# Kernel tuning notes

Measured on AMD Instinct MI355X. Metric: run time of the kernel, lower is better.

## Reference

```python
import jax, jax.numpy as jnp
import numpy as np

B, D_IN, T = 16, 1024, 4096
CB_SIZE, CB_DIM = 1024, 8
EPS = 1e-12  # F.normalize eps


def _wn_weight(v, g):
    # weight_norm over dim=0: per-output-row normalization. v: [out, in], g: [out]
    return g[:, None] * v / jnp.linalg.norm(v, axis=1, keepdims=True)


def setup_inputs() -> dict:
    key = jax.random.key(0)
    ks = jax.random.split(key, 8)
    z = jax.random.normal(ks[0], (B, D_IN, T), dtype=jnp.float32)
    in_v = jax.random.normal(ks[1], (CB_DIM, D_IN), dtype=jnp.float32) * 0.02
    in_g = jnp.linalg.norm(in_v, axis=1)  # weight_norm init: g = ||v||
    in_b = jnp.zeros((CB_DIM,), dtype=jnp.float32)
    out_v = jax.random.normal(ks[2], (D_IN, CB_DIM), dtype=jnp.float32) * 0.02
    out_g = jnp.linalg.norm(out_v, axis=1)
    out_b = jnp.zeros((D_IN,), dtype=jnp.float32)
    codebook = jax.random.normal(ks[3], (CB_SIZE, CB_DIM), dtype=jnp.float32)
    return {"z": z, "in_v": in_v, "in_g": in_g, "in_b": in_b,
            "out_v": out_v, "out_g": out_g, "out_b": out_b, "codebook": codebook}


def reference(z, in_v, in_g, in_b, out_v, out_g, out_b, codebook):
    # in_proj: 1x1 weight-normed conv, z: [B, D_IN, T] -> z_e: [B, CB_DIM, T]
    w_in = _wn_weight(in_v, in_g)
    z_e = jnp.einsum('od,bdt->bot', w_in, z) + in_b[None, :, None]

    # decode_latents: (b t) d tokens, L2-normalize, cosine distance, argmin
    enc = z_e.transpose(0, 2, 1).reshape(-1, CB_DIM)              # [(B*T), CB_DIM]
    enc_n = enc / jnp.maximum(jnp.linalg.norm(enc, axis=1, keepdims=True), EPS)
    cb_n = codebook / jnp.maximum(jnp.linalg.norm(codebook, axis=1, keepdims=True), EPS)
    dist = (jnp.sum(enc_n ** 2, axis=1, keepdims=True)
            - 2.0 * enc_n @ cb_n.T
            + jnp.sum(cb_n ** 2, axis=1)[None, :])                # [(B*T), CB_SIZE]
    indices = jnp.argmax(-dist, axis=1).reshape(B, T)             # argmin of dist
    z_q = codebook[indices].transpose(0, 2, 1)                    # [B, CB_DIM, T]

    commitment_loss = jnp.mean((z_e - jax.lax.stop_gradient(z_q)) ** 2, axis=(1, 2))
    codebook_loss = jnp.mean((z_q - jax.lax.stop_gradient(z_e)) ** 2, axis=(1, 2))

    # straight-through estimator
    z_q_st = z_e + jax.lax.stop_gradient(z_q - z_e)

    # out_proj: 1x1 weight-normed conv back to input_dim
    w_out = _wn_weight(out_v, out_g)
    z_out = jnp.einsum('od,bdt->bot', w_out, z_q_st) + out_b[None, :, None]
    return (z_out, commitment_loss, codebook_loss, indices, z_e)
```

## Files before the change

### kernel.cpp

```cpp
#include <hip/hip_runtime.h>
#include <math.h>


namespace {
constexpr int kB  = 16;
constexpr int kD  = 1024;
constexpr int kT  = 4096;
constexpr int kCB = 1024;
constexpr int kC  = 8;
constexpr float kEps = 1e-12f;

constexpr size_t N_ZOUT    = (size_t)kB * kD * kT;
constexpr size_t OFF_COMMIT = N_ZOUT;
constexpr size_t OFF_CBL    = OFF_COMMIT + kB;
constexpr size_t OFF_IDX    = OFF_CBL + kB;
constexpr size_t OFF_ZE     = OFF_IDX + (size_t)kB * kT;
}

__global__ void vq_prep(const float* __restrict__ in_v, const float* __restrict__ in_g,
                        const float* __restrict__ out_v, const float* __restrict__ out_g,
                        const float* __restrict__ cb,
                        float* __restrict__ w_in_t, float* __restrict__ w_out_t,
                        float* __restrict__ cb_n_t)
{
    __shared__ float red[4];
    const int blk = blockIdx.x;
    const int tid = threadIdx.x;
    if (blk < 8) {
        const int o = blk;
        float ss = 0.f;
        for (int d = tid; d < kD; d += 256) {
            float v = in_v[o * kD + d];
            ss = fmaf(v, v, ss);
        }
        #pragma unroll
        for (int off = 32; off; off >>= 1) ss += __shfl_xor(ss, off);
        if ((tid & 63) == 0) red[tid >> 6] = ss;
        __syncthreads();
        const float scale = in_g[o] / sqrtf(red[0] + red[1] + red[2] + red[3]);
        for (int d = tid; d < kD; d += 256)
            w_in_t[d * kC + o] = scale * in_v[o * kD + d];
    } else if (blk < 12) {
        const int r = (blk - 8) * 256 + tid;
        float4 a = reinterpret_cast<const float4*>(cb)[2 * r];
        float4 b = reinterpret_cast<const float4*>(cb)[2 * r + 1];
        float n = sqrtf(a.x*a.x + a.y*a.y + a.z*a.z + a.w*a.w +
                        b.x*b.x + b.y*b.y + b.z*b.z + b.w*b.w);
        float s = 1.f / fmaxf(n, kEps);
        a.x *= s; a.y *= s; a.z *= s; a.w *= s;
        b.x *= s; b.y *= s; b.z *= s; b.w *= s;
        reinterpret_cast<float4*>(cb_n_t)[2 * r]     = a;
        reinterpret_cast<float4*>(cb_n_t)[2 * r + 1] = b;
    } else {
        const int r = (blk - 12) * 256 + tid;
        float4 a = reinterpret_cast<const float4*>(out_v)[2 * r];
        float4 b = reinterpret_cast<const float4*>(out_v)[2 * r + 1];
        float n = sqrtf(a.x*a.x + a.y*a.y + a.z*a.z + a.w*a.w +
                        b.x*b.x + b.y*b.y + b.z*b.z + b.w*b.w);
        float s = out_g[r] / n;
        a.x *= s; a.y *= s; a.z *= s; a.w *= s;
        b.x *= s; b.y *= s; b.z *= s; b.w *= s;
        reinterpret_cast<float4*>(w_out_t)[2 * r]     = a;
        reinterpret_cast<float4*>(w_out_t)[2 * r + 1] = b;
    }
}

__global__ __launch_bounds__(256, 4)
void vq_main(const float* __restrict__ z,
             const float* __restrict__ in_b, const float* __restrict__ out_b,
             const float* __restrict__ cb,
             const float* __restrict__ w_in_t, const float* __restrict__ w_out_t,
             const float* __restrict__ cb_n_t,
             float* __restrict__ out)
{
    __shared__ float s_acc[4][kC][64];
    __shared__ float s_ze[kC][64];
    __shared__ float s_zq[kC][64];
    __shared__ float s_sim[4][64];
    __shared__ int   s_idx[4][64];

    const int tid = threadIdx.x;
    const int tx = tid & 63;
    const int ty = tid >> 6;
    const int g0 = blockIdx.x * 64;
    const int b  = g0 >> 12;
    const int t0 = g0 & (kT - 1);

    const float* zp = z + ((size_t)b * kD + (size_t)ty * 256) * kT + t0 + tx;
    const float4* wq = reinterpret_cast<const float4*>(w_in_t + (size_t)ty * 256 * kC);
    float acc[kC];
    #pragma unroll
    for (int c = 0; c < kC; c++) acc[c] = 0.f;

    #pragma unroll 4
    for (int i = 0; i < 256; i++) {
        float zv = zp[(size_t)i * kT];
        float4 w0 = wq[2 * i];
        float4 w1 = wq[2 * i + 1];
        acc[0] = fmaf(zv, w0.x, acc[0]);
        acc[1] = fmaf(zv, w0.y, acc[1]);
        acc[2] = fmaf(zv, w0.z, acc[2]);
        acc[3] = fmaf(zv, w0.w, acc[3]);
        acc[4] = fmaf(zv, w1.x, acc[4]);
        acc[5] = fmaf(zv, w1.y, acc[5]);
        acc[6] = fmaf(zv, w1.z, acc[6]);
        acc[7] = fmaf(zv, w1.w, acc[7]);
    }
    #pragma unroll
    for (int c = 0; c < kC; c++) s_acc[ty][c][tx] = acc[c];
    __syncthreads();

    #pragma unroll
    for (int cc = 0; cc < 2; cc++) {
        const int c = ty * 2 + cc;
        float v = s_acc[0][c][tx] + s_acc[1][c][tx] + s_acc[2][c][tx] + s_acc[3][c][tx]
                + in_b[c];
        s_ze[c][tx] = v;
    }
    __syncthreads();

    float ze[kC];
    #pragma unroll
    for (int c = 0; c < kC; c++) ze[c] = s_ze[c][tx];

    float best = -INFINITY;
    int bk = 0;
    const float4* cq = reinterpret_cast<const float4*>(cb_n_t + (size_t)ty * 256 * kC);
    #pragma unroll 2
    for (int j = 0; j < 256; j++) {
        float4 c0 = cq[2 * j];
        float4 c1 = cq[2 * j + 1];
        float sim = ze[0] * c0.x;
        sim = fmaf(ze[1], c0.y, sim);
        sim = fmaf(ze[2], c0.z, sim);
        sim = fmaf(ze[3], c0.w, sim);
        sim = fmaf(ze[4], c1.x, sim);
        sim = fmaf(ze[5], c1.y, sim);
        sim = fmaf(ze[6], c1.z, sim);
        sim = fmaf(ze[7], c1.w, sim);
        if (sim > best) { best = sim; bk = ty * 256 + j; }
    }
    s_sim[ty][tx] = best;
    s_idx[ty][tx] = bk;
    __syncthreads();

    if (ty == 0) {
        float bs = s_sim[0][tx];
        int   bi = s_idx[0][tx];
        #pragma unroll
        for (int g = 1; g < 4; g++) {
            float v = s_sim[g][tx];
            if (v > bs) { bs = v; bi = s_idx[g][tx]; }
        }
        out[OFF_IDX + (size_t)b * kT + t0 + tx] = (float)bi;

        float4 q0 = reinterpret_cast<const float4*>(cb)[2 * bi];
        float4 q1 = reinterpret_cast<const float4*>(cb)[2 * bi + 1];
        float zq[kC] = {q0.x, q0.y, q0.z, q0.w, q1.x, q1.y, q1.z, q1.w};

        float lsum = 0.f;
        #pragma unroll
        for (int c = 0; c < kC; c++) {
            s_zq[c][tx] = zq[c];
            float d = ze[c] - zq[c];
            lsum = fmaf(d, d, lsum);
            out[OFF_ZE + (size_t)b * (kC * kT) + (size_t)c * kT + t0 + tx] = ze[c];
        }
        #pragma unroll
        for (int off = 32; off; off >>= 1) lsum += __shfl_xor(lsum, off);
        if (tx == 0) {
            const float lv = lsum * (1.f / (kC * kT));
            atomicAdd(&out[OFF_COMMIT + b], lv);
            atomicAdd(&out[OFF_CBL + b], lv);
        }
    }
    __syncthreads();

    float zq[kC];
    #pragma unroll
    for (int c = 0; c < kC; c++) zq[c] = s_zq[c][tx];

    const int o0 = ty * 256;
    const float4* wo = reinterpret_cast<const float4*>(w_out_t + (size_t)o0 * kC);
    float* outp = out + ((size_t)b * kD + o0) * kT + t0 + tx;
    #pragma unroll 4
    for (int j = 0; j < 256; j++) {
        float4 w0 = wo[2 * j];
        float4 w1 = wo[2 * j + 1];
        float r = out_b[o0 + j];
        r = fmaf(zq[0], w0.x, r);
        r = fmaf(zq[1], w0.y, r);
        r = fmaf(zq[2], w0.z, r);
        r = fmaf(zq[3], w0.w, r);
        r = fmaf(zq[4], w1.x, r);
        r = fmaf(zq[5], w1.y, r);
        r = fmaf(zq[6], w1.z, r);
        r = fmaf(zq[7], w1.w, r);
        outp[(size_t)j * kT] = r;
    }
}

extern "C" void kernel_launch(void* const* d_in, const int* in_sizes, int n_in,
                              void* d_out, int out_size, void* d_ws, size_t ws_size,
                              hipStream_t stream) {
    const float* z     = (const float*)d_in[0];
    const float* in_v  = (const float*)d_in[1];
    const float* in_g  = (const float*)d_in[2];
    const float* in_b  = (const float*)d_in[3];
    const float* out_v = (const float*)d_in[4];
    const float* out_g = (const float*)d_in[5];
    const float* out_b = (const float*)d_in[6];
    const float* cb    = (const float*)d_in[7];
    float* out = (float*)d_out;

    float* w_in_t  = (float*)d_ws;
    float* w_out_t = w_in_t + (size_t)kD * kC;
    float* cb_n_t  = w_out_t + (size_t)kD * kC;

    vq_prep<<<16, 256, 0, stream>>>(in_v, in_g, out_v, out_g, cb,
                                    w_in_t, w_out_t, cb_n_t);
    hipMemsetAsync(out + OFF_COMMIT, 0, 2 * kB * sizeof(float), stream);
    vq_main<<<(kB * kT) / 64, 256, 0, stream>>>(z, in_b, out_b, cb,
                                                w_in_t, w_out_t, cb_n_t, out);
}
```

Measured before the change: 603.2 us.

## Remap vq_main threads to 4 tokens each with float4 loads and stores

Reassigns work so each thread handles 4 consecutive time steps across 16 slices of the reduction or codebook dimension, instead of one time step across 4 slices. The in-projection now uses float4 loads of z and reduces partials through wave shuffles plus shared memory. The codebook search and out-projection reuse each loaded weight or codebook row across 4 tokens and write float4 stores. This aims to cut weight and codebook load traffic per FMA and widen memory transactions on the bandwidth-bound z read and z_out write, at the cost of more registers (32 accumulators, 4x8 token arrays), which may lower occupancy under launch_bounds(256,4).

```diff
diff --git a/kernel.cpp b/kernel.cpp
--- a/kernel.cpp
+++ b/kernel.cpp
@@ -73,102 +73,126 @@
              const float* __restrict__ cb_n_t,
              float* __restrict__ out)
 {
-    __shared__ float s_acc[4][kC][64];
+    __shared__ float s_red[4][kC][64];
     __shared__ float s_ze[kC][64];
     __shared__ float s_zq[kC][64];
-    __shared__ float s_sim[4][64];
-    __shared__ int   s_idx[4][64];
+    __shared__ float s_sim[16][64];
+    __shared__ int   s_idx[16][64];
 
     const int tid = threadIdx.x;
-    const int tx = tid & 63;
-    const int ty = tid >> 6;
+    const int tg = tid & 15;
+    const int sl = tid >> 4;
+    const int wv = tid >> 6;
     const int g0 = blockIdx.x * 64;
     const int b  = g0 >> 12;
     const int t0 = g0 & (kT - 1);
 
-    const float* zp = z + ((size_t)b * kD + (size_t)ty * 256) * kT + t0 + tx;
-    const float4* wq = reinterpret_cast<const float4*>(w_in_t + (size_t)ty * 256 * kC);
-    float acc[kC];
-    #pragma unroll
-    for (int c = 0; c < kC; c++) acc[c] = 0.f;
+    const float* zp = z + ((size_t)b * kD + (size_t)sl * 64) * kT + t0 + 4 * tg;
+    const float4* wq = reinterpret_cast<const float4*>(w_in_t) + (size_t)sl * 128;
+    float acc[kC][4];
+    #pragma unroll
+    for (int c = 0; c < kC; c++)
+        #pragma unroll
+        for (int j = 0; j < 4; j++) acc[c][j] = 0.f;
 
     #pragma unroll 4
-    for (int i = 0; i < 256; i++) {
-        float zv = zp[(size_t)i * kT];
-        float4 w0 = wq[2 * i];
-        float4 w1 = wq[2 * i + 1];
-        acc[0] = fmaf(zv, w0.x, acc[0]);
-        acc[1] = fmaf(zv, w0.y, acc[1]);
-        acc[2] = fmaf(zv, w0.z, acc[2]);
-        acc[3] = fmaf(zv, w0.w, acc[3]);
-        acc[4] = fmaf(zv, w1.x, acc[4]);
-        acc[5] = fmaf(zv, w1.y, acc[5]);
-        acc[6] = fmaf(zv, w1.z, acc[6]);
-        acc[7] = fmaf(zv, w1.w, acc[7]);
-    }
-    #pragma unroll
-    for (int c = 0; c < kC; c++) s_acc[ty][c][tx] = acc[c];
-    __syncthreads();
-
-    #pragma unroll
-    for (int cc = 0; cc < 2; cc++) {
-        const int c = ty * 2 + cc;
-        float v = s_acc[0][c][tx] + s_acc[1][c][tx] + s_acc[2][c][tx] + s_acc[3][c][tx]
-                + in_b[c];
-        s_ze[c][tx] = v;
-    }
-    __syncthreads();
-
-    float ze[kC];
-    #pragma unroll
-    for (int c = 0; c < kC; c++) ze[c] = s_ze[c][tx];
-
-    float best = -INFINITY;
-    int bk = 0;
-    const float4* cq = reinterpret_cast<const float4*>(cb_n_t + (size_t)ty * 256 * kC);
+    for (int i = 0; i < 64; i++) {
+        const float4 zv = *reinterpret_cast<const float4*>(zp + (size_t)i * kT);
+        const float4 w0 = wq[2 * i];
+        const float4 w1 = wq[2 * i + 1];
+        const float zl[4] = {zv.x, zv.y, zv.z, zv.w};
+        const float wl[kC] = {w0.x, w0.y, w0.z, w0.w, w1.x, w1.y, w1.z, w1.w};
+        #pragma unroll
+        for (int c = 0; c < kC; c++)
+            #pragma unroll
+            for (int j = 0; j < 4; j++)
+                acc[c][j] = fmaf(zl[j], wl[c], acc[c][j]);
+    }
+    #pragma unroll
+    for (int c = 0; c < kC; c++)
+        #pragma unroll
+        for (int j = 0; j < 4; j++) {
+            float v = acc[c][j];
+            v += __shfl_xor(v, 16);
+            v += __shfl_xor(v, 32);
+            acc[c][j] = v;
+        }
+    if ((tid & 48) == 0) {
+        #pragma unroll
+        for (int c = 0; c < kC; c++)
+            #pragma unroll
+            for (int j = 0; j < 4; j++) s_red[wv][c][4 * tg + j] = acc[c][j];
+    }
+    __syncthreads();
+
+    {
+        const int c  = tid >> 5;
+        const int t2 = (tid & 31) * 2;
+        #pragma unroll
+        for (int k = 0; k < 2; k++) {
+            const int t = t2 + k;
+            s_ze[c][t] = s_red[0][c][t] + s_red[1][c][t] + s_red[2][c][t]
+                       + s_red[3][c][t] + in_b[c];
+        }
+    }
+    __syncthreads();
+
+    float zef[4][kC];
+    #pragma unroll
+    for (int j = 0; j < 4; j++)
+        #pragma unroll
+        for (int c = 0; c < kC; c++) zef[j][c] = s_ze[c][4 * tg + j];
+
+    float best[4] = {-INFINITY, -INFINITY, -INFINITY, -INFINITY};
+    int   bk[4]   = {sl * 64, sl * 64, sl * 64, sl * 64};
+    const float4* cq = reinterpret_cast<const float4*>(cb_n_t) + (size_t)sl * 128;
     #pragma unroll 2
-    for (int j = 0; j < 256; j++) {
-        float4 c0 = cq[2 * j];
-        float4 c1 = cq[2 * j + 1];
-        float sim = ze[0] * c0.x;
-        sim = fmaf(ze[1], c0.y, sim);
-        sim = fmaf(ze[2], c0.z, sim);
-        sim = fmaf(ze[3], c0.w, sim);
-        sim = fmaf(ze[4], c1.x, sim);
-        sim = fmaf(ze[5], c1.y, sim);
-        sim = fmaf(ze[6], c1.z, sim);
-        sim = fmaf(ze[7], c1.w, sim);
-        if (sim > best) { best = sim; bk = ty * 256 + j; }
-    }
-    s_sim[ty][tx] = best;
-    s_idx[ty][tx] = bk;
-    __syncthreads();
-
-    if (ty == 0) {
-        float bs = s_sim[0][tx];
-        int   bi = s_idx[0][tx];
-        #pragma unroll
-        for (int g = 1; g < 4; g++) {
-            float v = s_sim[g][tx];
-            if (v > bs) { bs = v; bi = s_idx[g][tx]; }
-        }
-        out[OFF_IDX + (size_t)b * kT + t0 + tx] = (float)bi;
-
-        float4 q0 = reinterpret_cast<const float4*>(cb)[2 * bi];
-        float4 q1 = reinterpret_cast<const float4*>(cb)[2 * bi + 1];
-        float zq[kC] = {q0.x, q0.y, q0.z, q0.w, q1.x, q1.y, q1.z, q1.w};
+    for (int i = 0; i < 64; i++) {
+        const float4 c0 = cq[2 * i];
+        const float4 c1 = cq[2 * i + 1];
+        const float cl[kC] = {c0.x, c0.y, c0.z, c0.w, c1.x, c1.y, c1.z, c1.w};
+        #pragma unroll
+        for (int j = 0; j < 4; j++) {
+            float sim = zef[j][0] * cl[0];
+            #pragma unroll
+            for (int c = 1; c < kC; c++) sim = fmaf(zef[j][c], cl[c], sim);
+            if (sim > best[j]) { best[j] = sim; bk[j] = sl * 64 + i; }
+        }
+    }
+    #pragma unroll
+    for (int j = 0; j < 4; j++) {
+        s_sim[sl][4 * tg + j] = best[j];
+        s_idx[sl][4 * tg + j] = bk[j];
+    }
+    __syncthreads();
+
+    if (tid < 64) {
+        const int t = tid;
+        float bs = s_sim[0][t];
+        int   bi = s_idx[0][t];
+        #pragma unroll
+        for (int g = 1; g < 16; g++) {
+            const float v = s_sim[g][t];
+            if (v > bs) { bs = v; bi = s_idx[g][t]; }
+        }
+        out[OFF_IDX + (size_t)b * kT + t0 + t] = (float)bi;
+
+        const float4 q0 = reinterpret_cast<const float4*>(cb)[2 * bi];
+        const float4 q1 = reinterpret_cast<const float4*>(cb)[2 * bi + 1];
+        const float zq[kC] = {q0.x, q0.y, q0.z, q0.w, q1.x, q1.y, q1.z, q1.w};
 
         float lsum = 0.f;
         #pragma unroll
         for (int c = 0; c < kC; c++) {
-            s_zq[c][tx] = zq[c];
-            float d = ze[c] - zq[c];
+            s_zq[c][t] = zq[c];
+            const float ze = s_ze[c][t];
+            const float d = ze - zq[c];
             lsum = fmaf(d, d, lsum);
-            out[OFF_ZE + (size_t)b * (kC * kT) + (size_t)c * kT + t0 + tx] = ze[c];
+            out[OFF_ZE + (size_t)b * (kC * kT) + (size_t)c * kT + t0 + t] = ze;
         }
         #pragma unroll
         for (int off = 32; off; off >>= 1) lsum += __shfl_xor(lsum, off);
-        if (tx == 0) {
+        if (tid == 0) {
             const float lv = lsum * (1.f / (kC * kT));
             atomicAdd(&out[OFF_COMMIT + b], lv);
             atomicAdd(&out[OFF_CBL + b], lv);
@@ -176,27 +200,31 @@
     }
     __syncthreads();
 
-    float zq[kC];
-    #pragma unroll
-    for (int c = 0; c < kC; c++) zq[c] = s_zq[c][tx];
-
-    const int o0 = ty * 256;
-    const float4* wo = reinterpret_cast<const float4*>(w_out_t + (size_t)o0 * kC);
-    float* outp = out + ((size_t)b * kD + o0) * kT + t0 + tx;
+    float zqr[4][kC];
+    #pragma unroll
+    for (int j = 0; j < 4; j++)
+        #pragma unroll
+        for (int c = 0; c < kC; c++) zqr[j][c] = s_zq[c][4 * tg + j];
+
+    const float4* wo = reinterpret_cast<const float4*>(w_out_t) + (size_t)sl * 128;
+    const float*  bo = out_b + sl * 64;
+    float* op = out + ((size_t)b * kD + (size_t)sl * 64) * kT + t0 + 4 * tg;
     #pragma unroll 4
-    for (int j = 0; j < 256; j++) {
-        float4 w0 = wo[2 * j];
-        float4 w1 = wo[2 * j + 1];
-        float r = out_b[o0 + j];
-        r = fmaf(zq[0], w0.x, r);
-        r = fmaf(zq[1], w0.y, r);
-        r = fmaf(zq[2], w0.z, r);
-        r = fmaf(zq[3], w0.w, r);
-        r = fmaf(zq[4], w1.x, r);
-        r = fmaf(zq[5], w1.y, r);
-        r = fmaf(zq[6], w1.z, r);
-        r = fmaf(zq[7], w1.w, r);
-        outp[(size_t)j * kT] = r;
+    for (int i = 0; i < 64; i++) {
+        const float4 w0 = wo[2 * i];
+        const float4 w1 = wo[2 * i + 1];
+        const float wl[kC] = {w0.x, w0.y, w0.z, w0.w, w1.x, w1.y, w1.z, w1.w};
+        const float bias = bo[i];
+        float rr[4];
+        #pragma unroll
+        for (int j = 0; j < 4; j++) {
+            float v = bias;
+            #pragma unroll
+            for (int c = 0; c < kC; c++) v = fmaf(zqr[j][c], wl[c], v);
+            rr[j] = v;
+        }
+        const float4 r = make_float4(rr[0], rr[1], rr[2], rr[3]);
+        *reinterpret_cast<float4*>(op + (size_t)i * kT) = r;
     }
 }
 
@@ -219,7 +247,7 @@
 
     vq_prep<<<16, 256, 0, stream>>>(in_v, in_g, out_v, out_g, cb,
                                     w_in_t, w_out_t, cb_n_t);
-    hipMemsetAsync(out + OFF_COMMIT, 0, 2 * kB * sizeof(float), stream);
+    (void)hipMemsetAsync(out + OFF_COMMIT, 0, 2 * kB * sizeof(float), stream);
     vq_main<<<(kB * kT) / 64, 256, 0, stream>>>(z, in_b, out_b, cb,
                                                 w_in_t, w_out_t, cb_n_t, out);
 }
```

Result: faster. 522.9 us (-13.3%).
